# Kernel tuning notes

Measured on AMD Instinct MI355X. Metric: run time of the kernel, lower is better.

The kernel has to match this reference:

```python
import jax, jax.numpy as jnp
import numpy as np

DILATION = 512
C_RES = 128
C_SKIP = 256


def setup_inputs() -> dict:
    key = jax.random.key(0)
    ks = jax.random.split(key, 6)
    B, T = 8, 16384
    x = jax.random.normal(ks[0], (B, C_RES, T), dtype=jnp.float32)
    # dilated conv weight: [out_ch, in_ch, kernel=2], no bias
    w_dil = jax.random.normal(ks[1], (C_RES, C_RES, 2), dtype=jnp.float32) * (1.0 / np.sqrt(2 * C_RES))
    # 1x1 residual conv (with bias)
    w_res = jax.random.normal(ks[2], (C_RES, C_RES), dtype=jnp.float32) * (1.0 / np.sqrt(C_RES))
    b_res = jax.random.normal(ks[3], (C_RES,), dtype=jnp.float32) * 0.01
    # 1x1 skip conv (with bias)
    w_skip = jax.random.normal(ks[4], (C_SKIP, C_RES), dtype=jnp.float32) * (1.0 / np.sqrt(C_RES))
    b_skip = jax.random.normal(ks[5], (C_SKIP,), dtype=jnp.float32) * 0.01
    return {"x": x, "w_dil": w_dil, "w_res": w_res, "b_res": b_res,
            "w_skip": w_skip, "b_skip": b_skip, "skip_size": 4096}


def reference(x, w_dil, w_res, b_res, w_skip, b_skip, skip_size):
    # x: [B, C, T]. Dilated causal conv, kernel_size=2, dilation=DILATION, no padding:
    # pre[:, :, t] = W[:,:,0] @ x[:,:,t] + W[:,:,1] @ x[:,:,t+DILATION], t in [0, T-DILATION)
    T = x.shape[2]
    L = T - DILATION  # output length
    pre = (jnp.einsum('oi,bit->bot', w_dil[:, :, 0], x[:, :, :L]) +
           jnp.einsum('oi,bit->bot', w_dil[:, :, 1], x[:, :, DILATION:]))
    activated = jnp.tanh(pre) * jax.nn.sigmoid(pre)  # filter * gate
    # 1x1 residual conv + residual add with the time-aligned tail of x
    out = (jnp.einsum('oi,bit->bot', w_res, activated) + b_res[None, :, None]
           + x[:, :, T - L:])
    # 1x1 skip conv, keep last skip_size steps
    skip = jnp.einsum('oi,bit->bot', w_skip, activated) + b_skip[None, :, None]
    skip = skip[:, :, -skip_size:]
    return (out, skip)
```

## Files before the change

kernel.cpp:

```cpp
#include <hip/hip_runtime.h>

typedef float f32x4 __attribute__((ext_vector_type(4)));
typedef __bf16 bf16x8 __attribute__((ext_vector_type(8)));

__device__ __forceinline__ unsigned short f2bf(float f) {
  unsigned u = __builtin_bit_cast(unsigned, f);
  u = (u + 0x7FFFu + ((u >> 16) & 1u)) >> 16;
  return (unsigned short)u;
}

__device__ __forceinline__ f32x4 MFMA16(uint4 a, uint4 b, f32x4 c) {
  return __builtin_amdgcn_mfma_f32_16x16x32_bf16(
      __builtin_bit_cast(bf16x8, a), __builtin_bit_cast(bf16x8, b), c, 0, 0, 0);
}

__global__ void wn_prep(const float* __restrict__ wd, const float* __restrict__ wres,
                        const float* __restrict__ wskip, unsigned short* __restrict__ ws16) {
  int g = blockIdx.x * 256 + threadIdx.x;
  if (g < 40960) {
    int kc = g / 5120, rem = g - kc * 5120;
    int o = rem / 40, c = rem - o * 40;
    float v = 0.f;
    if (c < 32) {
      int k = kc * 32 + c;
      int tap = k >> 7, i = k & 127;
      v = wd[(o << 8) + (i << 1) + tap];
    }
    ws16[g] = f2bf(v);
  } else {
    int g2 = g - 40960;
    int pkk = g2 >> 12;
    int rem = g2 & 4095;
    int o = rem >> 5, kl = rem & 31;
    int p = pkk >> 2, kk = pkk & 3;
    int k = kk * 32 + kl;
    float v = (p == 0) ? wres[o * 128 + k] : wskip[((p - 1) * 128 + o) * 128 + k];
    ws16[40960 + g2] = f2bf(v);
  }
}

__global__ __launch_bounds__(256, 4) void wn_main(
    const float* __restrict__ x,
    const float* __restrict__ bres_g,
    const float* __restrict__ bskip_g,
    const unsigned short* __restrict__ wd_img,
    const unsigned short* __restrict__ wrs2_img,
    float* __restrict__ out,
    float* __restrict__ skipo) {
  extern __shared__ unsigned short lds[];
  unsigned short* xls  = lds;
  unsigned short* actT = lds;
  unsigned short* wls  = lds + 8704;

  const int w = blockIdx.x;
  const int b = w & 7;
  const int tile = w >> 3;
  const int t0 = tile * 64;

  const int tid = threadIdx.x;
  const int lane = tid & 63;
  const int wv = tid >> 6;
  const int mw = wv >> 1;
  const int nw = wv & 1;
  const int l15 = lane & 15;
  const int lhi = lane >> 4;

  const int kq = tid & 7;
  const int tpr = tid >> 3;

  const float* xb_base = x + (size_t)b * (128 * 16384);

  float2 xr[4];
  uint4 wrA, wrB, wrC;

  auto issueX = [&](int kc) {
    int kglob = kc * 32 + kq * 4;
    int tap = kglob >> 7;
    int ib = kglob & 127;
    const float* p = xb_base + (size_t)ib * 16384 + (t0 + tap * 512 + tpr * 2);
    xr[0] = *(const float2*)(p);
    xr[1] = *(const float2*)(p + 16384);
    xr[2] = *(const float2*)(p + 32768);
    xr[3] = *(const float2*)(p + 49152);
  };
  auto writeX = [&](int buf) {
    unsigned short* dst = xls + buf * 2560;
    int r0 = tpr * 2;
    ushort4 a0, a1;
    a0.x = f2bf(xr[0].x); a0.y = f2bf(xr[1].x); a0.z = f2bf(xr[2].x); a0.w = f2bf(xr[3].x);
    a1.x = f2bf(xr[0].y); a1.y = f2bf(xr[1].y); a1.z = f2bf(xr[2].y); a1.w = f2bf(xr[3].y);
    *(ushort4*)(dst + r0 * 40 + kq * 4) = a0;
    *(ushort4*)(dst + (r0 + 1) * 40 + kq * 4) = a1;
  };
  auto loadW1 = [&](int kc) {
    const uint4* src = (const uint4*)(wd_img + kc * 5120);
    wrA = src[tid];
    wrB = src[tid + 256];
    if (tid < 128) wrC = src[tid + 512];
  };
  auto writeW1 = [&](int buf) {
    uint4* dst = (uint4*)(wls + buf * 5120);
    dst[tid] = wrA;
    dst[tid + 256] = wrB;
    if (tid < 128) dst[tid + 512] = wrC;
  };
  auto loadW2 = [&](int p, int kk) {
    const uint4* src = (const uint4*)(wrs2_img + ((p * 4 + kk) << 12));
    wrA = src[tid];
    wrB = src[tid + 256];
  };
  auto writeW2 = [&](int buf) {
    unsigned short* base = wls + buf * 5120;
    int u0 = tid, u1 = tid + 256;
    *(uint4*)(base + (u0 >> 2) * 40 + (u0 & 3) * 8) = wrA;
    *(uint4*)(base + (u1 >> 2) * 40 + (u1 & 3) * 8) = wrB;
  };

  f32x4 acc[4][2];
#pragma unroll
  for (int i = 0; i < 4; ++i)
#pragma unroll
    for (int j = 0; j < 2; ++j) acc[i][j] = (f32x4){0.f, 0.f, 0.f, 0.f};

  issueX(0); loadW1(0);
  writeX(0); writeW1(0);
  __syncthreads();

#pragma unroll
  for (int kc = 0; kc < 8; ++kc) {
    const int buf = kc & 1;
    if (kc < 7) { issueX(kc + 1); loadW1(kc + 1); }
    const unsigned short* wbuf = wls + buf * 5120;
    const unsigned short* xbuf = xls + buf * 2560;
    uint4 af[4], bfr[2];
#pragma unroll
    for (int mi = 0; mi < 4; ++mi)
      af[mi] = *(const uint4*)(wbuf + (mw * 64 + mi * 16 + l15) * 40 + lhi * 8);
#pragma unroll
    for (int ni = 0; ni < 2; ++ni)
      bfr[ni] = *(const uint4*)(xbuf + (nw * 32 + ni * 16 + l15) * 40 + lhi * 8);
#pragma unroll
    for (int mi = 0; mi < 4; ++mi)
#pragma unroll
      for (int ni = 0; ni < 2; ++ni)
        acc[mi][ni] = MFMA16(af[mi], bfr[ni], acc[mi][ni]);
    if (kc < 7) { writeX(buf ^ 1); writeW1(buf ^ 1); }
    __syncthreads();
  }

#pragma unroll
  for (int mi = 0; mi < 4; ++mi) {
#pragma unroll
    for (int ni = 0; ni < 2; ++ni) {
      ushort4 av;
#pragma unroll
      for (int r = 0; r < 4; ++r) {
        float p = acc[mi][ni][r];
        p = fminf(fmaxf(p, -15.f), 15.f);
        float ep = __expf(p);
        float e2 = ep * ep;
        float sg = ep * __builtin_amdgcn_rcpf(1.f + ep);
        float th = (e2 - 1.f) * __builtin_amdgcn_rcpf(e2 + 1.f);
        ((unsigned short*)&av)[r] = f2bf(th * sg);
      }
      int trow = nw * 32 + ni * 16 + l15;
      int o0 = mw * 64 + mi * 16 + lhi * 4;
      *(ushort4*)(actT + trow * 136 + o0) = av;
    }
  }

  const int npass = (tile >= 184) ? 3 : 1;
  for (int p = 0; p < npass; ++p) {
    loadW2(p, 0);
    writeW2(0);
    __syncthreads();

    f32x4 acc2[4][2];
#pragma unroll
    for (int i = 0; i < 4; ++i)
#pragma unroll
      for (int j = 0; j < 2; ++j) acc2[i][j] = (f32x4){0.f, 0.f, 0.f, 0.f};

#pragma unroll
    for (int kk = 0; kk < 4; ++kk) {
      const int buf = kk & 1;
      if (kk < 3) loadW2(p, kk + 1);
      const unsigned short* wbuf = wls + buf * 5120;
      uint4 af[4], bfr[2];
#pragma unroll
      for (int mi = 0; mi < 4; ++mi)
        af[mi] = *(const uint4*)(wbuf + (mw * 64 + mi * 16 + l15) * 40 + lhi * 8);
#pragma unroll
      for (int ni = 0; ni < 2; ++ni)
        bfr[ni] = *(const uint4*)(actT + (nw * 32 + ni * 16 + l15) * 136 + kk * 32 + lhi * 8);
#pragma unroll
      for (int mi = 0; mi < 4; ++mi)
#pragma unroll
        for (int ni = 0; ni < 2; ++ni)
          acc2[mi][ni] = MFMA16(af[mi], bfr[ni], acc2[mi][ni]);
      if (kk < 3) writeW2(buf ^ 1);
      __syncthreads();
    }

    if (p == 0) {
#pragma unroll
      for (int mi = 0; mi < 4; ++mi) {
        int o0 = mw * 64 + mi * 16 + lhi * 4;
        float br[4];
#pragma unroll
        for (int r = 0; r < 4; ++r) br[r] = bres_g[o0 + r];
#pragma unroll
        for (int ni = 0; ni < 2; ++ni) {
          int tl = nw * 32 + ni * 16 + l15;
#pragma unroll
          for (int r = 0; r < 4; ++r) {
            size_t row = (size_t)(b * 128 + o0 + r);
            float v = acc2[mi][ni][r] + br[r] + x[row * 16384 + 512 + t0 + tl];
            out[row * 15872 + t0 + tl] = v;
          }
        }
      }
    } else {
#pragma unroll
      for (int mi = 0; mi < 4; ++mi) {
        int o2 = (p - 1) * 128 + mw * 64 + mi * 16 + lhi * 4;
        float bs[4];
#pragma unroll
        for (int r = 0; r < 4; ++r) bs[r] = bskip_g[o2 + r];
#pragma unroll
        for (int ni = 0; ni < 2; ++ni) {
          int tl = nw * 32 + ni * 16 + l15;
          int s = t0 + tl - 11776;
#pragma unroll
          for (int r = 0; r < 4; ++r) {
            skipo[(size_t)(b * 256 + o2 + r) * 4096 + s] = acc2[mi][ni][r] + bs[r];
          }
        }
      }
    }
  }
}

extern "C" void kernel_launch(void* const* d_in, const int* in_sizes, int n_in,
                              void* d_out, int out_size, void* d_ws, size_t ws_size,
                              hipStream_t stream) {
  const float* x      = (const float*)d_in[0];
  const float* w_dil  = (const float*)d_in[1];
  const float* w_res  = (const float*)d_in[2];
  const float* b_res  = (const float*)d_in[3];
  const float* w_skip = (const float*)d_in[4];
  const float* b_skip = (const float*)d_in[5];
  unsigned short* ws16 = (unsigned short*)d_ws;
  float* out = (float*)d_out;
  float* skipo = out + 16252928;

  wn_prep<<<352, 256, 0, stream>>>(w_dil, w_res, w_skip, ws16);

  wn_main<<<1984, 256, 37888, stream>>>(x, b_res, b_skip, ws16, ws16 + 40960, out, skipo);
}
```

Measured before the change: 81.94 us.

## Stage the whole x tile into LDS up front and change LDS row padding

```diff
diff --git a/kernel.cpp b/kernel.cpp
--- a/kernel.cpp
+++ b/kernel.cpp
@@ -48,9 +48,9 @@
     float* __restrict__ out,
     float* __restrict__ skipo) {
   extern __shared__ unsigned short lds[];
-  unsigned short* xls  = lds;
+  unsigned short* xall = lds;
+  unsigned short* wls  = lds + 18432;
   unsigned short* actT = lds;
-  unsigned short* wls  = lds + 8704;
 
   const int w = blockIdx.x;
   const int b = w & 7;
@@ -70,28 +70,29 @@
 
   const float* xb_base = x + (size_t)b * (128 * 16384);
 
-  float2 xr[4];
-  uint4 wrA, wrB, wrC;
-
-  auto issueX = [&](int kc) {
+  float2 xr[4][4];
+
+  auto issueX = [&](int kc, int s) {
     int kglob = kc * 32 + kq * 4;
     int tap = kglob >> 7;
     int ib = kglob & 127;
     const float* p = xb_base + (size_t)ib * 16384 + (t0 + tap * 512 + tpr * 2);
-    xr[0] = *(const float2*)(p);
-    xr[1] = *(const float2*)(p + 16384);
-    xr[2] = *(const float2*)(p + 32768);
-    xr[3] = *(const float2*)(p + 49152);
-  };
-  auto writeX = [&](int buf) {
-    unsigned short* dst = xls + buf * 2560;
+    xr[s][0] = *(const float2*)(p);
+    xr[s][1] = *(const float2*)(p + 16384);
+    xr[s][2] = *(const float2*)(p + 32768);
+    xr[s][3] = *(const float2*)(p + 49152);
+  };
+  auto writeX = [&](int kc, int s) {
+    unsigned short* dst = xall + kc * 2304;
     int r0 = tpr * 2;
     ushort4 a0, a1;
-    a0.x = f2bf(xr[0].x); a0.y = f2bf(xr[1].x); a0.z = f2bf(xr[2].x); a0.w = f2bf(xr[3].x);
-    a1.x = f2bf(xr[0].y); a1.y = f2bf(xr[1].y); a1.z = f2bf(xr[2].y); a1.w = f2bf(xr[3].y);
-    *(ushort4*)(dst + r0 * 40 + kq * 4) = a0;
-    *(ushort4*)(dst + (r0 + 1) * 40 + kq * 4) = a1;
-  };
+    a0.x = f2bf(xr[s][0].x); a0.y = f2bf(xr[s][1].x); a0.z = f2bf(xr[s][2].x); a0.w = f2bf(xr[s][3].x);
+    a1.x = f2bf(xr[s][0].y); a1.y = f2bf(xr[s][1].y); a1.z = f2bf(xr[s][2].y); a1.w = f2bf(xr[s][3].y);
+    *(ushort4*)(dst + r0 * 36 + kq * 4) = a0;
+    *(ushort4*)(dst + (r0 + 1) * 36 + kq * 4) = a1;
+  };
+
+  uint4 wrA, wrB, wrC;
   auto loadW1 = [&](int kc) {
     const uint4* src = (const uint4*)(wd_img + kc * 5120);
     wrA = src[tid];
@@ -122,29 +123,37 @@
 #pragma unroll
     for (int j = 0; j < 2; ++j) acc[i][j] = (f32x4){0.f, 0.f, 0.f, 0.f};
 
-  issueX(0); loadW1(0);
-  writeX(0); writeW1(0);
+#pragma unroll
+  for (int c = 0; c < 4; ++c) issueX(c, c);
+  loadW1(0);
+#pragma unroll
+  for (int c = 0; c < 4; ++c) writeX(c, c);
+  writeW1(0);
+#pragma unroll
+  for (int c = 0; c < 4; ++c) issueX(4 + c, c);
+#pragma unroll
+  for (int c = 0; c < 4; ++c) writeX(4 + c, c);
   __syncthreads();
 
 #pragma unroll
   for (int kc = 0; kc < 8; ++kc) {
     const int buf = kc & 1;
-    if (kc < 7) { issueX(kc + 1); loadW1(kc + 1); }
+    if (kc < 7) loadW1(kc + 1);
     const unsigned short* wbuf = wls + buf * 5120;
-    const unsigned short* xbuf = xls + buf * 2560;
+    const unsigned short* xbuf = xall + kc * 2304;
     uint4 af[4], bfr[2];
 #pragma unroll
     for (int mi = 0; mi < 4; ++mi)
       af[mi] = *(const uint4*)(wbuf + (mw * 64 + mi * 16 + l15) * 40 + lhi * 8);
 #pragma unroll
     for (int ni = 0; ni < 2; ++ni)
-      bfr[ni] = *(const uint4*)(xbuf + (nw * 32 + ni * 16 + l15) * 40 + lhi * 8);
+      bfr[ni] = *(const uint4*)(xbuf + (nw * 32 + ni * 16 + l15) * 36 + lhi * 8);
 #pragma unroll
     for (int mi = 0; mi < 4; ++mi)
 #pragma unroll
       for (int ni = 0; ni < 2; ++ni)
         acc[mi][ni] = MFMA16(af[mi], bfr[ni], acc[mi][ni]);
-    if (kc < 7) { writeX(buf ^ 1); writeW1(buf ^ 1); }
+    if (kc < 7) writeW1(buf ^ 1);
     __syncthreads();
   }
 
@@ -165,7 +174,7 @@
       }
       int trow = nw * 32 + ni * 16 + l15;
       int o0 = mw * 64 + mi * 16 + lhi * 4;
-      *(ushort4*)(actT + trow * 136 + o0) = av;
+      *(ushort4*)(actT + trow * 140 + o0) = av;
     }
   }
 
@@ -192,7 +201,7 @@
         af[mi] = *(const uint4*)(wbuf + (mw * 64 + mi * 16 + l15) * 40 + lhi * 8);
 #pragma unroll
       for (int ni = 0; ni < 2; ++ni)
-        bfr[ni] = *(const uint4*)(actT + (nw * 32 + ni * 16 + l15) * 136 + kk * 32 + lhi * 8);
+        bfr[ni] = *(const uint4*)(actT + (nw * 32 + ni * 16 + l15) * 140 + kk * 32 + lhi * 8);
 #pragma unroll
       for (int mi = 0; mi < 4; ++mi)
 #pragma unroll
@@ -256,5 +265,5 @@
 
   wn_prep<<<352, 256, 0, stream>>>(w_dil, w_res, w_skip, ws16);
 
-  wn_main<<<1984, 256, 37888, stream>>>(x, b_res, b_skip, ws16, ws16 + 40960, out, skipo);
-}
+  wn_main<<<1984, 256, 57344, stream>>>(x, b_res, b_skip, ws16, ws16 + 40960, out, skipo);
+}
```

Result: slower. 109.0 us (+33.0%).
